# Kernel optimization log

Hardware: AMD Instinct MI355X
Metric: run time of the kernel (lower is better)

## Reference

```python
import jax, jax.numpy as jnp
import numpy as np

N_NODES = 100000
NUM_GRAPHS = 128
FEAT = 128
NUM_CLASSES = 4


def setup_inputs() -> dict:
    key = jax.random.key(0)
    ks = jax.random.split(key, 12)
    x = jax.random.normal(ks[0], (N_NODES, FEAT), dtype=jnp.float32)
    edge_index = jax.random.randint(ks[1], (2, 3200000), 0, N_NODES, dtype=jnp.int64)
    batch = jnp.sort(jax.random.randint(ks[2], (N_NODES,), 0, NUM_GRAPHS, dtype=jnp.int64))

    def glorot(k, fan_in, fan_out):
        lim = float(np.sqrt(6.0 / (fan_in + fan_out)))
        return jax.random.uniform(k, (fan_in, fan_out), jnp.float32, -lim, lim)

    dims = [FEAT, 16, 32, 64, NUM_CLASSES]
    params = {}
    for i in range(4):
        params[f"W{i+1}"] = glorot(ks[3 + i], dims[i], dims[i + 1])
        params[f"b{i+1}"] = jnp.zeros((dims[i + 1],), jnp.float32)
    return dict(x=x, edge_index=edge_index, batch=batch, **params)


def _gcn_norm(edge_index, n):
    # add self-loops, then symmetric normalization deg^{-1/2} A_hat deg^{-1/2}
    loop = jnp.arange(n, dtype=edge_index.dtype)
    row = jnp.concatenate([edge_index[0], loop])  # source
    col = jnp.concatenate([edge_index[1], loop])  # target
    deg = jax.ops.segment_sum(jnp.ones_like(col, jnp.float32), col, num_segments=n)
    dinv = jnp.where(deg > 0, jax.lax.rsqrt(deg), 0.0)
    norm = dinv[row] * dinv[col]  # [E+N]
    return row, col, norm


def _gcn_conv(x, row, col, norm, W, b):
    h = x @ W  # [N, out]
    msg = h[row] * norm[:, None]  # gather + scale, [E+N, out]
    agg = jax.ops.segment_sum(msg, col, num_segments=x.shape[0])
    return agg + b


def reference(x, edge_index, batch, W1, b1, W2, b2, W3, b3, W4, b4):
    n = x.shape[0]
    row, col, norm = _gcn_norm(edge_index, n)
    # dropout is identity in eval mode
    h = jax.nn.relu(_gcn_conv(x, row, col, norm, W1, b1))
    h = jax.nn.relu(_gcn_conv(h, row, col, norm, W2, b2))
    h = jax.nn.relu(_gcn_conv(h, row, col, norm, W3, b3))
    h = _gcn_conv(h, row, col, norm, W4, b4)
    pooled = jax.ops.segment_max(h, batch, num_segments=NUM_GRAPHS)  # [G, C]
    return jax.nn.log_softmax(pooled, axis=1)
```

## Files before the change

kernel.cpp:

```cpp
#include <hip/hip_runtime.h>

#define DIV_UP(a,b) (((a)+(b)-1)/(b))

constexpr int BSHIFT = 7;
constexpr int BNODES = 128;
constexpr int CHUNK_E = 16384;
constexpr int PTH = 512;
constexpr int SCH = 8;
constexpr int SCSH = 14;

__device__ inline unsigned short f2bf(float f) {
    unsigned u = __float_as_uint(f);
    u = u + 0x7FFFu + ((u >> 16) & 1u);
    return (unsigned short)(u >> 16);
}
__device__ inline float bflo(unsigned u) { return __uint_as_float(u << 16); }
__device__ inline float bfhi(unsigned u) { return __uint_as_float(u & 0xFFFF0000u); }

__global__ void zero_int_k(int* p, int n) {
    int i = blockIdx.x * blockDim.x + threadIdx.x;
    if (i < n) p[i] = 0;
}

__global__ void bucket_hist_k(const int* __restrict__ col, int* __restrict__ bhist, int E, int nb) {
    __shared__ int lh[1024];
    for (int i = threadIdx.x; i < 1024; i += blockDim.x) lh[i] = 0;
    __syncthreads();
    int stride = gridDim.x * blockDim.x;
    for (int e = blockIdx.x * blockDim.x + threadIdx.x; e < E; e += stride)
        atomicAdd(&lh[col[e] >> BSHIFT], 1);
    __syncthreads();
    for (int i = threadIdx.x; i < nb; i += blockDim.x) {
        int v = lh[i];
        if (v) atomicAdd(&bhist[i], v);
    }
}

__global__ void bucket_scan_k(const int* __restrict__ bhist, int* __restrict__ bcur, int nb) {
    __shared__ int lds[256];
    int base = threadIdx.x * 4;
    int v[4]; int s = 0;
#pragma unroll
    for (int j = 0; j < 4; j++) { v[j] = (base + j < nb) ? bhist[base + j] : 0; s += v[j]; }
    lds[threadIdx.x] = s; __syncthreads();
    for (int off = 1; off < 256; off <<= 1) {
        int t = (threadIdx.x >= off) ? lds[threadIdx.x - off] : 0;
        __syncthreads();
        lds[threadIdx.x] += t;
        __syncthreads();
    }
    int excl = lds[threadIdx.x] - s;
#pragma unroll
    for (int j = 0; j < 4; j++) {
        if (base + j < nb) bcur[base + j] = excl;
        excl += v[j];
    }
}

__global__ void __launch_bounds__(PTH) partition_k(
        const int* __restrict__ row, const int* __restrict__ col,
        int* __restrict__ bcur, int* __restrict__ part, int E, int nb) {
    __shared__ int lh[1024];
    __shared__ int lbase[1024];
    __shared__ int delta[1024];
    __shared__ unsigned sorted[CHUNK_E];
    __shared__ unsigned short bid[CHUNK_E];
    int tid = threadIdx.x;
    for (int i = tid; i < 1024; i += PTH) lh[i] = 0;
    __syncthreads();
    int base = blockIdx.x * CHUNK_E;
    int end = min(E, base + CHUNK_E);
    for (int e = base + tid; e < end; e += PTH)
        atomicAdd(&lh[col[e] >> BSHIFT], 1);
    __syncthreads();
    int v0 = lh[2 * tid], v1 = lh[2 * tid + 1];
    int s = v0 + v1;
    delta[tid] = s;
    __syncthreads();
    for (int off = 1; off < PTH; off <<= 1) {
        int t = (tid >= off) ? delta[tid - off] : 0;
        __syncthreads();
        delta[tid] += t;
        __syncthreads();
    }
    int excl = delta[tid] - s;
    lbase[2 * tid] = excl;
    lbase[2 * tid + 1] = excl + v0;
    __syncthreads();
    for (int i = tid; i < nb; i += PTH) {
        int c = lh[i];
        int g = c ? atomicAdd(&bcur[i], c) : 0;
        delta[i] = g - lbase[i];
    }
    __syncthreads();
    for (int i = tid; i < nb; i += PTH) lh[i] = lbase[i];
    __syncthreads();
    for (int e = base + tid; e < end; e += PTH) {
        int r = row[e], c = col[e];
        int b = c >> BSHIFT;
        int slot = atomicAdd(&lh[b], 1);
        sorted[slot] = (unsigned)((r << BSHIFT) | (c & (BNODES - 1)));
        bid[slot] = (unsigned short)b;
    }
    __syncthreads();
    int cnt = end - base;
    for (int i = tid; i < cnt; i += PTH) {
        int b = bid[i];
        part[delta[b] + i] = (int)sorted[i];
    }
}

__global__ void __launch_bounds__(256) csr_build_k(
        const int* __restrict__ part, const int* __restrict__ bcur,
        int* __restrict__ cur, float* __restrict__ dinv,
        int* __restrict__ csr, int N) {
    __shared__ int cnt[BNODES * SCH];
    __shared__ int scan_t[256];
    __shared__ int ebounds[2];
    int b = blockIdx.x;
    int tid = threadIdx.x;
    if (tid == 0) { ebounds[0] = b ? bcur[b - 1] : 0; ebounds[1] = bcur[b]; }
    for (int i = tid; i < BNODES * SCH; i += 256) cnt[i] = 0;
    __syncthreads();
    int e0 = ebounds[0], e1 = ebounds[1];
    for (int e = e0 + tid; e < e1; e += 256) {
        unsigned v = (unsigned)part[e];
        int cell = (int)(v & (BNODES - 1)) * SCH + (int)(v >> (BSHIFT + SCSH));
        atomicAdd(&cnt[cell], 1);
    }
    __syncthreads();
    int base4 = tid * 4;
    int c0 = cnt[base4], c1 = cnt[base4+1], c2 = cnt[base4+2], c3 = cnt[base4+3];
    int s = c0 + c1 + c2 + c3;
    scan_t[tid] = s;
    __syncthreads();
    for (int off = 1; off < 256; off <<= 1) {
        int t = (tid >= off) ? scan_t[tid - off] : 0;
        __syncthreads();
        scan_t[tid] += t;
        __syncthreads();
    }
    int excl = scan_t[tid] - s;
    cnt[base4]     = excl;
    cnt[base4 + 1] = excl + c0;
    cnt[base4 + 2] = excl + c0 + c1;
    cnt[base4 + 3] = excl + c0 + c1 + c2;
    __syncthreads();
    if (tid < BNODES) {
        int node = b * BNODES + tid;
        int segstart = cnt[tid * SCH];
        int segend   = (tid == BNODES - 1) ? (e1 - e0) : cnt[(tid + 1) * SCH];
        if (node < N) {
            cur[node]  = e0 + segend;
            dinv[node] = rsqrtf(1.0f + (float)(segend - segstart));
        }
    }
    __syncthreads();
    for (int e = e0 + tid; e < e1; e += 256) {
        unsigned v = (unsigned)part[e];
        int cell = (int)(v & (BNODES - 1)) * SCH + (int)(v >> (BSHIFT + SCSH));
        int p = atomicAdd(&cnt[cell], 1);
        csr[e0 + p] = (int)(v >> BSHIFT);
    }
}

__global__ void __launch_bounds__(256) gather16_bf_k(
        const unsigned short* __restrict__ hb, const float* __restrict__ dinv,
        const int* __restrict__ cur, const int* __restrict__ csr,
        const float* __restrict__ b, unsigned short* __restrict__ outb, int n) {
    int t2 = blockIdx.x * 256 + threadIdx.x;
    int node = t2 >> 1, t = t2 & 1;
    if (node >= n) return;
    const uint4* hb4 = reinterpret_cast<const uint4*>(hb);
    uint4 sv = hb4[(size_t)node * 2 + t];
    float a0 = bflo(sv.x), a1 = bfhi(sv.x), a2 = bflo(sv.y), a3 = bfhi(sv.y);
    float a4 = bflo(sv.z), a5 = bfhi(sv.z), a6 = bflo(sv.w), a7 = bfhi(sv.w);
    int e0 = node ? cur[node - 1] : 0;
    int e1 = cur[node];
    int e = e0;
    for (; e + 3 < e1; e += 4) {
        int s0 = csr[e], s1 = csr[e+1], s2 = csr[e+2], s3 = csr[e+3];
        uint4 v0 = hb4[(size_t)s0 * 2 + t];
        uint4 v1 = hb4[(size_t)s1 * 2 + t];
        uint4 v2 = hb4[(size_t)s2 * 2 + t];
        uint4 v3 = hb4[(size_t)s3 * 2 + t];
        a0 += (bflo(v0.x) + bflo(v1.x)) + (bflo(v2.x) + bflo(v3.x));
        a1 += (bfhi(v0.x) + bfhi(v1.x)) + (bfhi(v2.x) + bfhi(v3.x));
        a2 += (bflo(v0.y) + bflo(v1.y)) + (bflo(v2.y) + bflo(v3.y));
        a3 += (bfhi(v0.y) + bfhi(v1.y)) + (bfhi(v2.y) + bfhi(v3.y));
        a4 += (bflo(v0.z) + bflo(v1.z)) + (bflo(v2.z) + bflo(v3.z));
        a5 += (bfhi(v0.z) + bfhi(v1.z)) + (bfhi(v2.z) + bfhi(v3.z));
        a6 += (bflo(v0.w) + bflo(v1.w)) + (bflo(v2.w) + bflo(v3.w));
        a7 += (bfhi(v0.w) + bfhi(v1.w)) + (bfhi(v2.w) + bfhi(v3.w));
    }
    for (; e < e1; e++) {
        uint4 v = hb4[(size_t)csr[e] * 2 + t];
        a0 += bflo(v.x); a1 += bfhi(v.x); a2 += bflo(v.y); a3 += bfhi(v.y);
        a4 += bflo(v.z); a5 += bfhi(v.z); a6 += bflo(v.w); a7 += bfhi(v.w);
    }
    float di = dinv[node];
    int bo = t * 8;
    a0 = fmaxf(a0 * di + b[bo+0], 0.f) * di; a1 = fmaxf(a1 * di + b[bo+1], 0.f) * di;
    a2 = fmaxf(a2 * di + b[bo+2], 0.f) * di; a3 = fmaxf(a3 * di + b[bo+3], 0.f) * di;
    a4 = fmaxf(a4 * di + b[bo+4], 0.f) * di; a5 = fmaxf(a5 * di + b[bo+5], 0.f) * di;
    a6 = fmaxf(a6 * di + b[bo+6], 0.f) * di; a7 = fmaxf(a7 * di + b[bo+7], 0.f) * di;
    uint4 pk;
    pk.x = (unsigned)f2bf(a0) | ((unsigned)f2bf(a1) << 16);
    pk.y = (unsigned)f2bf(a2) | ((unsigned)f2bf(a3) << 16);
    pk.z = (unsigned)f2bf(a4) | ((unsigned)f2bf(a5) << 16);
    pk.w = (unsigned)f2bf(a6) | ((unsigned)f2bf(a7) << 16);
    reinterpret_cast<uint4*>(outb)[(size_t)node * 2 + t] = pk;
}

__global__ void __launch_bounds__(256) gmm16_32_k(
        const unsigned short* __restrict__ hb, const float* __restrict__ dinv,
        const int* __restrict__ cur, const int* __restrict__ csr,
        const float* __restrict__ W, const float* __restrict__ b,
        unsigned short* __restrict__ yb, int n) {
    constexpr int TN = 128, RS = 20;
    __shared__ float xs[TN * RS];
    __shared__ float Ws[16 * 32];
    __shared__ float bs[32];
    for (int i = threadIdx.x; i < 16 * 32; i += 256) Ws[i] = W[i];
    if (threadIdx.x < 32) bs[threadIdx.x] = b[threadIdx.x];
    int base = blockIdx.x * TN;
    {
        int nl = threadIdx.x >> 1, t = threadIdx.x & 1;
        int node = base + nl;
        if (node < n) {
            const uint4* hb4 = reinterpret_cast<const uint4*>(hb);
            uint4 sv = hb4[(size_t)node * 2 + t];
            float a0 = bflo(sv.x), a1 = bfhi(sv.x), a2 = bflo(sv.y), a3 = bfhi(sv.y);
            float a4 = bflo(sv.z), a5 = bfhi(sv.z), a6 = bflo(sv.w), a7 = bfhi(sv.w);
            int e0 = node ? cur[node - 1] : 0;
            int e1 = cur[node];
            int e = e0;
            for (; e + 3 < e1; e += 4) {
                int s0 = csr[e], s1 = csr[e+1], s2 = csr[e+2], s3 = csr[e+3];
                uint4 v0 = hb4[(size_t)s0 * 2 + t];
                uint4 v1 = hb4[(size_t)s1 * 2 + t];
                uint4 v2 = hb4[(size_t)s2 * 2 + t];
                uint4 v3 = hb4[(size_t)s3 * 2 + t];
                a0 += (bflo(v0.x) + bflo(v1.x)) + (bflo(v2.x) + bflo(v3.x));
                a1 += (bfhi(v0.x) + bfhi(v1.x)) + (bfhi(v2.x) + bfhi(v3.x));
                a2 += (bflo(v0.y) + bflo(v1.y)) + (bflo(v2.y) + bflo(v3.y));
                a3 += (bfhi(v0.y) + bfhi(v1.y)) + (bfhi(v2.y) + bfhi(v3.y));
                a4 += (bflo(v0.z) + bflo(v1.z)) + (bflo(v2.z) + bflo(v3.z));
                a5 += (bfhi(v0.z) + bfhi(v1.z)) + (bfhi(v2.z) + bfhi(v3.z));
                a6 += (bflo(v0.w) + bflo(v1.w)) + (bflo(v2.w) + bflo(v3.w));
                a7 += (bfhi(v0.w) + bfhi(v1.w)) + (bfhi(v2.w) + bfhi(v3.w));
            }
            for (; e < e1; e++) {
                uint4 v = hb4[(size_t)csr[e] * 2 + t];
                a0 += bflo(v.x); a1 += bfhi(v.x); a2 += bflo(v.y); a3 += bfhi(v.y);
                a4 += bflo(v.z); a5 += bfhi(v.z); a6 += bflo(v.w); a7 += bfhi(v.w);
            }
            float di = dinv[node];
            float* dst = &xs[nl * RS + t * 8];
            dst[0] = a0*di; dst[1] = a1*di; dst[2] = a2*di; dst[3] = a3*di;
            dst[4] = a4*di; dst[5] = a5*di; dst[6] = a6*di; dst[7] = a7*di;
        }
    }
    __syncthreads();
    int nl = threadIdx.x >> 1, g = threadIdx.x & 1;
    int node = base + nl;
    if (node >= n) return;
    int j0 = g * 16;
    float acc[16];
#pragma unroll
    for (int j = 0; j < 16; j++) acc[j] = 0.f;
    const float* xrow = &xs[nl * RS];
#pragma unroll
    for (int k4 = 0; k4 < 4; k4++) {
        float4 xv = *reinterpret_cast<const float4*>(&xrow[k4 * 4]);
        float xk[4] = {xv.x, xv.y, xv.z, xv.w};
#pragma unroll
        for (int kk = 0; kk < 4; kk++) {
            const float* wrow = &Ws[(k4*4+kk) * 32 + j0];
#pragma unroll
            for (int j = 0; j < 16; j++) acc[j] += xk[kk] * wrow[j];
        }
    }
    float di = dinv[node];
    unsigned short* yr = yb + (size_t)node * 32 + j0;
#pragma unroll
    for (int q = 0; q < 2; q++) {
        float o[8];
#pragma unroll
        for (int j = 0; j < 8; j++)
            o[j] = fmaxf(acc[q*8+j] + bs[j0 + q*8 + j], 0.f) * di;
        uint4 pk;
        pk.x = (unsigned)f2bf(o[0]) | ((unsigned)f2bf(o[1]) << 16);
        pk.y = (unsigned)f2bf(o[2]) | ((unsigned)f2bf(o[3]) << 16);
        pk.z = (unsigned)f2bf(o[4]) | ((unsigned)f2bf(o[5]) << 16);
        pk.w = (unsigned)f2bf(o[6]) | ((unsigned)f2bf(o[7]) << 16);
        reinterpret_cast<uint4*>(yr)[q] = pk;
    }
}

__global__ void __launch_bounds__(256) gmm32_64_k(
        const unsigned short* __restrict__ hb, const float* __restrict__ dinv,
        const int* __restrict__ cur, const int* __restrict__ csr,
        const float* __restrict__ W, const float* __restrict__ b,
        unsigned short* __restrict__ yb, int n) {
    constexpr int TN = 64, RS = 36;
    __shared__ float xs[TN * RS];
    __shared__ float Ws[32 * 64];
    __shared__ float bs[64];
    for (int i = threadIdx.x; i < 32 * 64; i += 256) Ws[i] = W[i];
    if (threadIdx.x < 64) bs[threadIdx.x] = b[threadIdx.x];
    int base = blockIdx.x * TN;
    {
        int nl = threadIdx.x >> 2, t = threadIdx.x & 3;
        int node = base + nl;
        if (node < n) {
            const uint4* hb4 = reinterpret_cast<const uint4*>(hb);
            uint4 sv = hb4[(size_t)node * 4 + t];
            float a0 = bflo(sv.x), a1 = bfhi(sv.x), a2 = bflo(sv.y), a3 = bfhi(sv.y);
            float a4 = bflo(sv.z), a5 = bfhi(sv.z), a6 = bflo(sv.w), a7 = bfhi(sv.w);
            int e0 = node ? cur[node - 1] : 0;
            int e1 = cur[node];
            int e = e0;
            for (; e + 3 < e1; e += 4) {
                int s0 = csr[e], s1 = csr[e+1], s2 = csr[e+2], s3 = csr[e+3];
                uint4 v0 = hb4[(size_t)s0 * 4 + t];
                uint4 v1 = hb4[(size_t)s1 * 4 + t];
                uint4 v2 = hb4[(size_t)s2 * 4 + t];
                uint4 v3 = hb4[(size_t)s3 * 4 + t];
                a0 += (bflo(v0.x) + bflo(v1.x)) + (bflo(v2.x) + bflo(v3.x));
                a1 += (bfhi(v0.x) + bfhi(v1.x)) + (bfhi(v2.x) + bfhi(v3.x));
                a2 += (bflo(v0.y) + bflo(v1.y)) + (bflo(v2.y) + bflo(v3.y));
                a3 += (bfhi(v0.y) + bfhi(v1.y)) + (bfhi(v2.y) + bfhi(v3.y));
                a4 += (bflo(v0.z) + bflo(v1.z)) + (bflo(v2.z) + bflo(v3.z));
                a5 += (bfhi(v0.z) + bfhi(v1.z)) + (bfhi(v2.z) + bfhi(v3.z));
                a6 += (bflo(v0.w) + bflo(v1.w)) + (bflo(v2.w) + bflo(v3.w));
                a7 += (bfhi(v0.w) + bfhi(v1.w)) + (bfhi(v2.w) + bfhi(v3.w));
            }
            for (; e < e1; e++) {
                uint4 v = hb4[(size_t)csr[e] * 4 + t];
                a0 += bflo(v.x); a1 += bfhi(v.x); a2 += bflo(v.y); a3 += bfhi(v.y);
                a4 += bflo(v.z); a5 += bfhi(v.z); a6 += bflo(v.w); a7 += bfhi(v.w);
            }
            float di = dinv[node];
            float* dst = &xs[nl * RS + t * 8];
            dst[0] = a0*di; dst[1] = a1*di; dst[2] = a2*di; dst[3] = a3*di;
            dst[4] = a4*di; dst[5] = a5*di; dst[6] = a6*di; dst[7] = a7*di;
        }
    }
    __syncthreads();
    int nl = threadIdx.x >> 2, g = threadIdx.x & 3;
    int node = base + nl;
    if (node >= n) return;
    int j0 = g * 16;
    float acc[16];
#pragma unroll
    for (int j = 0; j < 16; j++) acc[j] = 0.f;
    const float* xrow = &xs[nl * RS];
#pragma unroll
    for (int k4 = 0; k4 < 8; k4++) {
        float4 xv = *reinterpret_cast<const float4*>(&xrow[k4 * 4]);
        float xk[4] = {xv.x, xv.y, xv.z, xv.w};
#pragma unroll
        for (int kk = 0; kk < 4; kk++) {
            const float* wrow = &Ws[(k4*4+kk) * 64 + j0];
#pragma unroll
            for (int j = 0; j < 16; j++) acc[j] += xk[kk] * wrow[j];
        }
    }
    float di = dinv[node];
    unsigned short* yr = yb + (size_t)node * 64 + j0;
#pragma unroll
    for (int q = 0; q < 2; q++) {
        float o[8];
#pragma unroll
        for (int j = 0; j < 8; j++)
            o[j] = fmaxf(acc[q*8+j] + bs[j0 + q*8 + j], 0.f) * di;
        uint4 pk;
        pk.x = (unsigned)f2bf(o[0]) | ((unsigned)f2bf(o[1]) << 16);
        pk.y = (unsigned)f2bf(o[2]) | ((unsigned)f2bf(o[3]) << 16);
        pk.z = (unsigned)f2bf(o[4]) | ((unsigned)f2bf(o[5]) << 16);
        pk.w = (unsigned)f2bf(o[6]) | ((unsigned)f2bf(o[7]) << 16);
        reinterpret_cast<uint4*>(yr)[q] = pk;
    }
}

__device__ inline unsigned fkey(float x) {
    unsigned u = __float_as_uint(x);
    return (u & 0x80000000u) ? ~u : (u | 0x80000000u);
}
__device__ inline float funkey(unsigned k) {
    unsigned u = (k & 0x80000000u) ? (k & 0x7FFFFFFFu) : ~k;
    return __uint_as_float(u);
}

__global__ void gather4_pool_k(const float* __restrict__ hs, const float* __restrict__ dinv,
                               const int* __restrict__ cur, const int* __restrict__ csr,
                               const float* __restrict__ b4, const int* __restrict__ batch,
                               unsigned* __restrict__ pooled, int n, int num_graphs) {
    __shared__ unsigned lds[128 * 4];
    for (int i = threadIdx.x; i < num_graphs * 4; i += blockDim.x) lds[i] = 0u;
    __syncthreads();
    int node = blockIdx.x * blockDim.x + threadIdx.x;
    if (node < n) {
        float di = dinv[node];
        float4 acc = reinterpret_cast<const float4*>(hs)[node];
        int e0 = node ? cur[node - 1] : 0;
        int e1 = cur[node];
        int e = e0;
        for (; e + 3 < e1; e += 4) {
            int s0 = csr[e], s1 = csr[e+1], s2 = csr[e+2], s3 = csr[e+3];
            float4 v0 = reinterpret_cast<const float4*>(hs)[s0];
            float4 v1 = reinterpret_cast<const float4*>(hs)[s1];
            float4 v2 = reinterpret_cast<const float4*>(hs)[s2];
            float4 v3 = reinterpret_cast<const float4*>(hs)[s3];
            acc.x += (v0.x + v1.x) + (v2.x + v3.x);
            acc.y += (v0.y + v1.y) + (v2.y + v3.y);
            acc.z += (v0.z + v1.z) + (v2.z + v3.z);
            acc.w += (v0.w + v1.w) + (v2.w + v3.w);
        }
        for (; e < e1; e++) {
            float4 v0 = reinterpret_cast<const float4*>(hs)[csr[e]];
            acc.x += v0.x; acc.y += v0.y; acc.z += v0.z; acc.w += v0.w;
        }
        int g = batch[node];
        atomicMax(&lds[g*4+0], fkey(acc.x * di + b4[0]));
        atomicMax(&lds[g*4+1], fkey(acc.y * di + b4[1]));
        atomicMax(&lds[g*4+2], fkey(acc.z * di + b4[2]));
        atomicMax(&lds[g*4+3], fkey(acc.w * di + b4[3]));
    }
    __syncthreads();
    for (int i2 = threadIdx.x; i2 < num_graphs * 4; i2 += blockDim.x) {
        unsigned k = lds[i2];
        if (k) atomicMax(&pooled[i2], k);
    }
}

__global__ void pool_init_k(unsigned* pooled, int total) {
    int i = blockIdx.x * blockDim.x + threadIdx.x;
    if (i < total) pooled[i] = 0u;
}

__global__ void logsoftmax_k(const unsigned* __restrict__ pooled, float* __restrict__ out, int G) {
    int g = blockIdx.x * blockDim.x + threadIdx.x;
    if (g >= G) return;
    float v[4];
#pragma unroll
    for (int j = 0; j < 4; j++) v[j] = funkey(pooled[g*4+j]);
    float m = fmaxf(fmaxf(v[0], v[1]), fmaxf(v[2], v[3]));
    float s = 0.f;
#pragma unroll
    for (int j = 0; j < 4; j++) s += expf(v[j] - m);
    float l = logf(s);
#pragma unroll
    for (int j = 0; j < 4; j++) out[g*4+j] = v[j] - m - l;
}

template<int IN, int OUT, bool RELU, bool BIAS, bool SCALE, bool IBF, bool OBF>
__global__ void __launch_bounds__(256) matmul_k(
        const void* __restrict__ xv, const float* __restrict__ W,
        const float* __restrict__ b, const float* __restrict__ dinv,
        void* __restrict__ yv, int n) {
    constexpr int TN  = 64;
    constexpr int RS  = IN + 4;
    constexpr int OPT = OUT / 4;
    constexpr int NQ  = IN / 4;
    __shared__ float xs[TN * RS];
    __shared__ float Ws[IN * OUT];
    __shared__ float bs[OUT];

    for (int i = threadIdx.x; i < IN * OUT; i += 256) Ws[i] = W[i];
    if (BIAS) for (int i = threadIdx.x; i < OUT; i += 256) bs[i] = b[i];

    int base = blockIdx.x * TN;
    if constexpr (!IBF) {
        const float* x = (const float*)xv;
        for (int i = threadIdx.x; i < TN * NQ; i += 256) {
            int r = i / NQ, c = i % NQ;
            float4 v = make_float4(0.f, 0.f, 0.f, 0.f);
            if (base + r < n) v = reinterpret_cast<const float4*>(x + (size_t)(base + r) * IN)[c];
            *reinterpret_cast<float4*>(&xs[r * RS + c * 4]) = v;
        }
    } else {
        constexpr int NU = IN / 8;
        const uint4* x = (const uint4*)xv;
        for (int i = threadIdx.x; i < TN * NU; i += 256) {
            int r = i / NU, c = i % NU;
            uint4 v = make_uint4(0u, 0u, 0u, 0u);
            if (base + r < n) v = x[(size_t)(base + r) * NU + c];
            float* dst = &xs[r * RS + c * 8];
            dst[0] = bflo(v.x); dst[1] = bfhi(v.x);
            dst[2] = bflo(v.y); dst[3] = bfhi(v.y);
            dst[4] = bflo(v.z); dst[5] = bfhi(v.z);
            dst[6] = bflo(v.w); dst[7] = bfhi(v.w);
        }
    }
    __syncthreads();

    int node = threadIdx.x >> 2;
    int g    = threadIdx.x & 3;
    int j0   = g * OPT;
    int gnode = base + node;
    if (gnode >= n) return;

    float acc[OPT];
#pragma unroll
    for (int jj = 0; jj < OPT; jj++) acc[jj] = 0.f;

    const float* xrow = &xs[node * RS];
#pragma unroll
    for (int k4 = 0; k4 < NQ; k4++) {
        float4 xvv = *reinterpret_cast<const float4*>(&xrow[k4 * 4]);
        float xk[4] = {xvv.x, xvv.y, xvv.z, xvv.w};
#pragma unroll
        for (int kk = 0; kk < 4; kk++) {
            const float* wrow = &Ws[(k4 * 4 + kk) * OUT + j0];
#pragma unroll
            for (int jj = 0; jj < OPT; jj++)
                acc[jj] += xk[kk] * wrow[jj];
        }
    }

    float di = SCALE ? dinv[gnode] : 1.f;
    float vout[OPT];
#pragma unroll
    for (int jj = 0; jj < OPT; jj++) {
        float v = acc[jj] + (BIAS ? bs[j0 + jj] : 0.f);
        if (RELU) v = fmaxf(v, 0.f);
        if (SCALE) v *= di;
        vout[jj] = v;
    }
    if constexpr (OBF) {
        unsigned short* yr = (unsigned short*)yv + (size_t)gnode * OUT + j0;
        if constexpr (OPT % 8 == 0) {
#pragma unroll
            for (int q = 0; q < OPT / 8; q++) {
                uint4 pk;
                pk.x = (unsigned)f2bf(vout[q*8+0]) | ((unsigned)f2bf(vout[q*8+1]) << 16);
                pk.y = (unsigned)f2bf(vout[q*8+2]) | ((unsigned)f2bf(vout[q*8+3]) << 16);
                pk.z = (unsigned)f2bf(vout[q*8+4]) | ((unsigned)f2bf(vout[q*8+5]) << 16);
                pk.w = (unsigned)f2bf(vout[q*8+6]) | ((unsigned)f2bf(vout[q*8+7]) << 16);
                reinterpret_cast<uint4*>(yr)[q] = pk;
            }
        } else {
            uint2 pk;
            pk.x = (unsigned)f2bf(vout[0]) | ((unsigned)f2bf(vout[1]) << 16);
            pk.y = (unsigned)f2bf(vout[2]) | ((unsigned)f2bf(vout[3]) << 16);
            *reinterpret_cast<uint2*>(yr) = pk;
        }
    } else {
        float* yr = (float*)yv + (size_t)gnode * OUT + j0;
        if (OPT % 4 == 0) {
#pragma unroll
            for (int q = 0; q < OPT / 4; q++)
                *reinterpret_cast<float4*>(yr + q * 4) =
                    make_float4(vout[q*4+0], vout[q*4+1], vout[q*4+2], vout[q*4+3]);
        } else {
#pragma unroll
            for (int jj = 0; jj < OPT; jj++) yr[jj] = vout[jj];
        }
    }
}

extern "C" void kernel_launch(void* const* d_in, const int* in_sizes, int n_in,
                              void* d_out, int out_size, void* d_ws, size_t ws_size,
                              hipStream_t stream) {
    const float* x     = (const float*)d_in[0];
    const int*   ei    = (const int*)d_in[1];
    const int*   batch = (const int*)d_in[2];
    const float* W1 = (const float*)d_in[3];
    const float* b1 = (const float*)d_in[4];
    const float* W2 = (const float*)d_in[5];
    const float* b2 = (const float*)d_in[6];
    const float* W3 = (const float*)d_in[7];
    const float* b3 = (const float*)d_in[8];
    const float* W4 = (const float*)d_in[9];
    const float* b4 = (const float*)d_in[10];

    const int N = in_sizes[2];
    const int E = in_sizes[1] / 2;
    const int G = 128;
    const int* row = ei;
    const int* col = ei + E;
    const int NB = DIV_UP(N, BNODES);

    float* ws    = (float*)d_ws;
    float* dinv  = ws;
    int*   cur   = (int*)(dinv + N);
    int*   bhist = cur + N;
    int*   bcur  = bhist + 1024;
    int*   csr   = bcur + 1024;
    float* f16a  = (float*)(csr + E);
    float* f16b  = f16a + (size_t)N * 16;
    float* f32a  = f16b + (size_t)N * 16;
    float* f32b  = f32a + (size_t)N * 32;
    unsigned* pooled = (unsigned*)(f32b + (size_t)N * 32);
    int* part = (int*)f32a;
    unsigned short* hb16a = (unsigned short*)f16a;
    unsigned short* hb16b = (unsigned short*)f16b;
    unsigned short* hb32  = (unsigned short*)f32a;
    unsigned short* hb64  = (unsigned short*)f32b;
    float* f4a = f16a;

    const int B = 256;
    const int gridN = DIV_UP(N, B);
    const int gridM = DIV_UP(N, 64);
    const int grid2 = DIV_UP(2 * N, B);
    const int gridF = DIV_UP(N, 128);

    zero_int_k<<<DIV_UP(1024, B), B, 0, stream>>>(bhist, 1024);
    bucket_hist_k<<<512, B, 0, stream>>>(col, bhist, E, NB);
    bucket_scan_k<<<1, 256, 0, stream>>>(bhist, bcur, NB);
    partition_k<<<DIV_UP(E, CHUNK_E), PTH, 0, stream>>>(row, col, bcur, part, E, NB);
    csr_build_k<<<NB, 256, 0, stream>>>(part, bcur, cur, dinv, csr, N);

    matmul_k<128,16,false,false,true,false,true><<<gridM, B, 0, stream>>>(x, W1, nullptr, dinv, hb16b, N);
    gather16_bf_k<<<grid2, B, 0, stream>>>(hb16b, dinv, cur, csr, b1, hb16a, N);

    gmm16_32_k<<<gridF, B, 0, stream>>>(hb16a, dinv, cur, csr, W2, b2, hb32, N);

    gmm32_64_k<<<gridM, B, 0, stream>>>(hb32, dinv, cur, csr, W3, b3, hb64, N);

    matmul_k<64,4,false,false,false,true,false><<<gridM, B, 0, stream>>>(hb64, W4, nullptr, nullptr, f4a, N);
    pool_init_k<<<DIV_UP(G*4, B), B, 0, stream>>>(pooled, G*4);
    gather4_pool_k<<<gridN, B, 0, stream>>>(f4a, dinv, cur, csr, b4, batch, pooled, N, G);

    logsoftmax_k<<<1, 128, 0, stream>>>(pooled, (float*)d_out, G);
}
```

Measured before the change: 228.2 us.

## Split each node's edge list across multiple lanes with shuffle reduction in gathers

All four neighbor-aggregation kernels now assign several lanes per node (4x, 2x, 2x and 8x respectively) that stride through the node's edge list and combine partial sums with xor shuffles. This raises the number of independent gather loads in flight and shortens per-thread serial loops, targeting latency-bound random gathers. Node tiles per block are halved in the fused GEMM kernels, and each thread computes 8 output columns instead of 16. The cost is more threads, extra shuffle work, and idle lanes on low-degree nodes.

```diff
diff --git a/kernel.cpp b/kernel.cpp
--- a/kernel.cpp
+++ b/kernel.cpp
@@ -168,22 +168,26 @@
         const unsigned short* __restrict__ hb, const float* __restrict__ dinv,
         const int* __restrict__ cur, const int* __restrict__ csr,
         const float* __restrict__ b, unsigned short* __restrict__ outb, int n) {
-    int t2 = blockIdx.x * 256 + threadIdx.x;
-    int node = t2 >> 1, t = t2 & 1;
+    int tid = blockIdx.x * 256 + threadIdx.x;
+    int node = tid >> 3, sub = tid & 7;
+    int rh = sub & 1, p = sub >> 1;
     if (node >= n) return;
     const uint4* hb4 = reinterpret_cast<const uint4*>(hb);
-    uint4 sv = hb4[(size_t)node * 2 + t];
-    float a0 = bflo(sv.x), a1 = bfhi(sv.x), a2 = bflo(sv.y), a3 = bfhi(sv.y);
-    float a4 = bflo(sv.z), a5 = bfhi(sv.z), a6 = bflo(sv.w), a7 = bfhi(sv.w);
+    float a0 = 0.f, a1 = 0.f, a2 = 0.f, a3 = 0.f, a4 = 0.f, a5 = 0.f, a6 = 0.f, a7 = 0.f;
+    if (p == 0) {
+        uint4 sv = hb4[(size_t)node * 2 + rh];
+        a0 = bflo(sv.x); a1 = bfhi(sv.x); a2 = bflo(sv.y); a3 = bfhi(sv.y);
+        a4 = bflo(sv.z); a5 = bfhi(sv.z); a6 = bflo(sv.w); a7 = bfhi(sv.w);
+    }
     int e0 = node ? cur[node - 1] : 0;
     int e1 = cur[node];
-    int e = e0;
-    for (; e + 3 < e1; e += 4) {
-        int s0 = csr[e], s1 = csr[e+1], s2 = csr[e+2], s3 = csr[e+3];
-        uint4 v0 = hb4[(size_t)s0 * 2 + t];
-        uint4 v1 = hb4[(size_t)s1 * 2 + t];
-        uint4 v2 = hb4[(size_t)s2 * 2 + t];
-        uint4 v3 = hb4[(size_t)s3 * 2 + t];
+    int e = e0 + p;
+    for (; e + 12 < e1; e += 16) {
+        int s0 = csr[e], s1 = csr[e+4], s2 = csr[e+8], s3 = csr[e+12];
+        uint4 v0 = hb4[(size_t)s0 * 2 + rh];
+        uint4 v1 = hb4[(size_t)s1 * 2 + rh];
+        uint4 v2 = hb4[(size_t)s2 * 2 + rh];
+        uint4 v3 = hb4[(size_t)s3 * 2 + rh];
         a0 += (bflo(v0.x) + bflo(v1.x)) + (bflo(v2.x) + bflo(v3.x));
         a1 += (bfhi(v0.x) + bfhi(v1.x)) + (bfhi(v2.x) + bfhi(v3.x));
         a2 += (bflo(v0.y) + bflo(v1.y)) + (bflo(v2.y) + bflo(v3.y));
@@ -193,13 +197,18 @@
         a6 += (bflo(v0.w) + bflo(v1.w)) + (bflo(v2.w) + bflo(v3.w));
         a7 += (bfhi(v0.w) + bfhi(v1.w)) + (bfhi(v2.w) + bfhi(v3.w));
     }
-    for (; e < e1; e++) {
-        uint4 v = hb4[(size_t)csr[e] * 2 + t];
+    for (; e < e1; e += 4) {
+        uint4 v = hb4[(size_t)csr[e] * 2 + rh];
         a0 += bflo(v.x); a1 += bfhi(v.x); a2 += bflo(v.y); a3 += bfhi(v.y);
         a4 += bflo(v.z); a5 += bfhi(v.z); a6 += bflo(v.w); a7 += bfhi(v.w);
     }
+    a0 += __shfl_xor(a0, 2); a1 += __shfl_xor(a1, 2); a2 += __shfl_xor(a2, 2); a3 += __shfl_xor(a3, 2);
+    a4 += __shfl_xor(a4, 2); a5 += __shfl_xor(a5, 2); a6 += __shfl_xor(a6, 2); a7 += __shfl_xor(a7, 2);
+    a0 += __shfl_xor(a0, 4); a1 += __shfl_xor(a1, 4); a2 += __shfl_xor(a2, 4); a3 += __shfl_xor(a3, 4);
+    a4 += __shfl_xor(a4, 4); a5 += __shfl_xor(a5, 4); a6 += __shfl_xor(a6, 4); a7 += __shfl_xor(a7, 4);
+    if (p != 0) return;
     float di = dinv[node];
-    int bo = t * 8;
+    int bo = rh * 8;
     a0 = fmaxf(a0 * di + b[bo+0], 0.f) * di; a1 = fmaxf(a1 * di + b[bo+1], 0.f) * di;
     a2 = fmaxf(a2 * di + b[bo+2], 0.f) * di; a3 = fmaxf(a3 * di + b[bo+3], 0.f) * di;
     a4 = fmaxf(a4 * di + b[bo+4], 0.f) * di; a5 = fmaxf(a5 * di + b[bo+5], 0.f) * di;
@@ -209,7 +218,7 @@
     pk.y = (unsigned)f2bf(a2) | ((unsigned)f2bf(a3) << 16);
     pk.z = (unsigned)f2bf(a4) | ((unsigned)f2bf(a5) << 16);
     pk.w = (unsigned)f2bf(a6) | ((unsigned)f2bf(a7) << 16);
-    reinterpret_cast<uint4*>(outb)[(size_t)node * 2 + t] = pk;
+    reinterpret_cast<uint4*>(outb)[(size_t)node * 2 + rh] = pk;
 }
 
 __global__ void __launch_bounds__(256) gmm16_32_k(
@@ -217,7 +226,7 @@
         const int* __restrict__ cur, const int* __restrict__ csr,
         const float* __restrict__ W, const float* __restrict__ b,
         unsigned short* __restrict__ yb, int n) {
-    constexpr int TN = 128, RS = 20;
+    constexpr int TN = 64, RS = 20;
     __shared__ float xs[TN * RS];
     __shared__ float Ws[16 * 32];
     __shared__ float bs[32];
@@ -225,22 +234,26 @@
     if (threadIdx.x < 32) bs[threadIdx.x] = b[threadIdx.x];
     int base = blockIdx.x * TN;
     {
-        int nl = threadIdx.x >> 1, t = threadIdx.x & 1;
+        int nl = threadIdx.x >> 2, sub = threadIdx.x & 3;
+        int rh = sub & 1, p = sub >> 1;
         int node = base + nl;
         if (node < n) {
             const uint4* hb4 = reinterpret_cast<const uint4*>(hb);
-            uint4 sv = hb4[(size_t)node * 2 + t];
-            float a0 = bflo(sv.x), a1 = bfhi(sv.x), a2 = bflo(sv.y), a3 = bfhi(sv.y);
-            float a4 = bflo(sv.z), a5 = bfhi(sv.z), a6 = bflo(sv.w), a7 = bfhi(sv.w);
+            float a0 = 0.f, a1 = 0.f, a2 = 0.f, a3 = 0.f, a4 = 0.f, a5 = 0.f, a6 = 0.f, a7 = 0.f;
+            if (p == 0) {
+                uint4 sv = hb4[(size_t)node * 2 + rh];
+                a0 = bflo(sv.x); a1 = bfhi(sv.x); a2 = bflo(sv.y); a3 = bfhi(sv.y);
+                a4 = bflo(sv.z); a5 = bfhi(sv.z); a6 = bflo(sv.w); a7 = bfhi(sv.w);
+            }
             int e0 = node ? cur[node - 1] : 0;
             int e1 = cur[node];
-            int e = e0;
-            for (; e + 3 < e1; e += 4) {
-                int s0 = csr[e], s1 = csr[e+1], s2 = csr[e+2], s3 = csr[e+3];
-                uint4 v0 = hb4[(size_t)s0 * 2 + t];
-                uint4 v1 = hb4[(size_t)s1 * 2 + t];
-                uint4 v2 = hb4[(size_t)s2 * 2 + t];
-                uint4 v3 = hb4[(size_t)s3 * 2 + t];
+            int e = e0 + p;
+            for (; e + 6 < e1; e += 8) {
+                int s0 = csr[e], s1 = csr[e+2], s2 = csr[e+4], s3 = csr[e+6];
+                uint4 v0 = hb4[(size_t)s0 * 2 + rh];
+                uint4 v1 = hb4[(size_t)s1 * 2 + rh];
+                uint4 v2 = hb4[(size_t)s2 * 2 + rh];
+                uint4 v3 = hb4[(size_t)s3 * 2 + rh];
                 a0 += (bflo(v0.x) + bflo(v1.x)) + (bflo(v2.x) + bflo(v3.x));
                 a1 += (bfhi(v0.x) + bfhi(v1.x)) + (bfhi(v2.x) + bfhi(v3.x));
                 a2 += (bflo(v0.y) + bflo(v1.y)) + (bflo(v2.y) + bflo(v3.y));
@@ -250,25 +263,29 @@
                 a6 += (bflo(v0.w) + bflo(v1.w)) + (bflo(v2.w) + bflo(v3.w));
                 a7 += (bfhi(v0.w) + bfhi(v1.w)) + (bfhi(v2.w) + bfhi(v3.w));
             }
-            for (; e < e1; e++) {
-                uint4 v = hb4[(size_t)csr[e] * 2 + t];
+            for (; e < e1; e += 2) {
+                uint4 v = hb4[(size_t)csr[e] * 2 + rh];
                 a0 += bflo(v.x); a1 += bfhi(v.x); a2 += bflo(v.y); a3 += bfhi(v.y);
                 a4 += bflo(v.z); a5 += bfhi(v.z); a6 += bflo(v.w); a7 += bfhi(v.w);
             }
-            float di = dinv[node];
-            float* dst = &xs[nl * RS + t * 8];
-            dst[0] = a0*di; dst[1] = a1*di; dst[2] = a2*di; dst[3] = a3*di;
-            dst[4] = a4*di; dst[5] = a5*di; dst[6] = a6*di; dst[7] = a7*di;
-        }
-    }
-    __syncthreads();
-    int nl = threadIdx.x >> 1, g = threadIdx.x & 1;
+            a0 += __shfl_xor(a0, 2); a1 += __shfl_xor(a1, 2); a2 += __shfl_xor(a2, 2); a3 += __shfl_xor(a3, 2);
+            a4 += __shfl_xor(a4, 2); a5 += __shfl_xor(a5, 2); a6 += __shfl_xor(a6, 2); a7 += __shfl_xor(a7, 2);
+            if (p == 0) {
+                float di = dinv[node];
+                float* dst = &xs[nl * RS + rh * 8];
+                dst[0] = a0*di; dst[1] = a1*di; dst[2] = a2*di; dst[3] = a3*di;
+                dst[4] = a4*di; dst[5] = a5*di; dst[6] = a6*di; dst[7] = a7*di;
+            }
+        }
+    }
+    __syncthreads();
+    int nl = threadIdx.x >> 2, g = threadIdx.x & 3;
     int node = base + nl;
     if (node >= n) return;
-    int j0 = g * 16;
-    float acc[16];
-#pragma unroll
-    for (int j = 0; j < 16; j++) acc[j] = 0.f;
+    int j0 = g * 8;
+    float acc[8];
+#pragma unroll
+    for (int j = 0; j < 8; j++) acc[j] = 0.f;
     const float* xrow = &xs[nl * RS];
 #pragma unroll
     for (int k4 = 0; k4 < 4; k4++) {
@@ -278,24 +295,19 @@
         for (int kk = 0; kk < 4; kk++) {
             const float* wrow = &Ws[(k4*4+kk) * 32 + j0];
 #pragma unroll
-            for (int j = 0; j < 16; j++) acc[j] += xk[kk] * wrow[j];
+            for (int j = 0; j < 8; j++) acc[j] += xk[kk] * wrow[j];
         }
     }
     float di = dinv[node];
-    unsigned short* yr = yb + (size_t)node * 32 + j0;
-#pragma unroll
-    for (int q = 0; q < 2; q++) {
-        float o[8];
-#pragma unroll
-        for (int j = 0; j < 8; j++)
-            o[j] = fmaxf(acc[q*8+j] + bs[j0 + q*8 + j], 0.f) * di;
-        uint4 pk;
-        pk.x = (unsigned)f2bf(o[0]) | ((unsigned)f2bf(o[1]) << 16);
-        pk.y = (unsigned)f2bf(o[2]) | ((unsigned)f2bf(o[3]) << 16);
-        pk.z = (unsigned)f2bf(o[4]) | ((unsigned)f2bf(o[5]) << 16);
-        pk.w = (unsigned)f2bf(o[6]) | ((unsigned)f2bf(o[7]) << 16);
-        reinterpret_cast<uint4*>(yr)[q] = pk;
-    }
+    float o[8];
+#pragma unroll
+    for (int j = 0; j < 8; j++) o[j] = fmaxf(acc[j] + bs[j0 + j], 0.f) * di;
+    uint4 pk;
+    pk.x = (unsigned)f2bf(o[0]) | ((unsigned)f2bf(o[1]) << 16);
+    pk.y = (unsigned)f2bf(o[2]) | ((unsigned)f2bf(o[3]) << 16);
+    pk.z = (unsigned)f2bf(o[4]) | ((unsigned)f2bf(o[5]) << 16);
+    pk.w = (unsigned)f2bf(o[6]) | ((unsigned)f2bf(o[7]) << 16);
+    *reinterpret_cast<uint4*>(yb + (size_t)node * 32 + j0) = pk;
 }
 
 __global__ void __launch_bounds__(256) gmm32_64_k(
@@ -303,7 +315,7 @@
         const int* __restrict__ cur, const int* __restrict__ csr,
         const float* __restrict__ W, const float* __restrict__ b,
         unsigned short* __restrict__ yb, int n) {
-    constexpr int TN = 64, RS = 36;
+    constexpr int TN = 32, RS = 36;
     __shared__ float xs[TN * RS];
     __shared__ float Ws[32 * 64];
     __shared__ float bs[64];
@@ -311,22 +323,26 @@
     if (threadIdx.x < 64) bs[threadIdx.x] = b[threadIdx.x];
     int base = blockIdx.x * TN;
     {
-        int nl = threadIdx.x >> 2, t = threadIdx.x & 3;
+        int nl = threadIdx.x >> 3, sub = threadIdx.x & 7;
+        int rq = sub & 3, p = sub >> 2;
         int node = base + nl;
         if (node < n) {
             const uint4* hb4 = reinterpret_cast<const uint4*>(hb);
-            uint4 sv = hb4[(size_t)node * 4 + t];
-            float a0 = bflo(sv.x), a1 = bfhi(sv.x), a2 = bflo(sv.y), a3 = bfhi(sv.y);
-            float a4 = bflo(sv.z), a5 = bfhi(sv.z), a6 = bflo(sv.w), a7 = bfhi(sv.w);
+            float a0 = 0.f, a1 = 0.f, a2 = 0.f, a3 = 0.f, a4 = 0.f, a5 = 0.f, a6 = 0.f, a7 = 0.f;
+            if (p == 0) {
+                uint4 sv = hb4[(size_t)node * 4 + rq];
+                a0 = bflo(sv.x); a1 = bfhi(sv.x); a2 = bflo(sv.y); a3 = bfhi(sv.y);
+                a4 = bflo(sv.z); a5 = bfhi(sv.z); a6 = bflo(sv.w); a7 = bfhi(sv.w);
+            }
             int e0 = node ? cur[node - 1] : 0;
             int e1 = cur[node];
-            int e = e0;
-            for (; e + 3 < e1; e += 4) {
-                int s0 = csr[e], s1 = csr[e+1], s2 = csr[e+2], s3 = csr[e+3];
-                uint4 v0 = hb4[(size_t)s0 * 4 + t];
-                uint4 v1 = hb4[(size_t)s1 * 4 + t];
-                uint4 v2 = hb4[(size_t)s2 * 4 + t];
-                uint4 v3 = hb4[(size_t)s3 * 4 + t];
+            int e = e0 + p;
+            for (; e + 6 < e1; e += 8) {
+                int s0 = csr[e], s1 = csr[e+2], s2 = csr[e+4], s3 = csr[e+6];
+                uint4 v0 = hb4[(size_t)s0 * 4 + rq];
+                uint4 v1 = hb4[(size_t)s1 * 4 + rq];
+                uint4 v2 = hb4[(size_t)s2 * 4 + rq];
+                uint4 v3 = hb4[(size_t)s3 * 4 + rq];
                 a0 += (bflo(v0.x) + bflo(v1.x)) + (bflo(v2.x) + bflo(v3.x));
                 a1 += (bfhi(v0.x) + bfhi(v1.x)) + (bfhi(v2.x) + bfhi(v3.x));
                 a2 += (bflo(v0.y) + bflo(v1.y)) + (bflo(v2.y) + bflo(v3.y));
@@ -336,25 +352,29 @@
                 a6 += (bflo(v0.w) + bflo(v1.w)) + (bflo(v2.w) + bflo(v3.w));
                 a7 += (bfhi(v0.w) + bfhi(v1.w)) + (bfhi(v2.w) + bfhi(v3.w));
             }
-            for (; e < e1; e++) {
-                uint4 v = hb4[(size_t)csr[e] * 4 + t];
+            for (; e < e1; e += 2) {
+                uint4 v = hb4[(size_t)csr[e] * 4 + rq];
                 a0 += bflo(v.x); a1 += bfhi(v.x); a2 += bflo(v.y); a3 += bfhi(v.y);
                 a4 += bflo(v.z); a5 += bfhi(v.z); a6 += bflo(v.w); a7 += bfhi(v.w);
             }
-            float di = dinv[node];
-            float* dst = &xs[nl * RS + t * 8];
-            dst[0] = a0*di; dst[1] = a1*di; dst[2] = a2*di; dst[3] = a3*di;
-            dst[4] = a4*di; dst[5] = a5*di; dst[6] = a6*di; dst[7] = a7*di;
-        }
-    }
-    __syncthreads();
-    int nl = threadIdx.x >> 2, g = threadIdx.x & 3;
+            a0 += __shfl_xor(a0, 4); a1 += __shfl_xor(a1, 4); a2 += __shfl_xor(a2, 4); a3 += __shfl_xor(a3, 4);
+            a4 += __shfl_xor(a4, 4); a5 += __shfl_xor(a5, 4); a6 += __shfl_xor(a6, 4); a7 += __shfl_xor(a7, 4);
+            if (p == 0) {
+                float di = dinv[node];
+                float* dst = &xs[nl * RS + rq * 8];
+                dst[0] = a0*di; dst[1] = a1*di; dst[2] = a2*di; dst[3] = a3*di;
+                dst[4] = a4*di; dst[5] = a5*di; dst[6] = a6*di; dst[7] = a7*di;
+            }
+        }
+    }
+    __syncthreads();
+    int nl = threadIdx.x >> 3, g = threadIdx.x & 7;
     int node = base + nl;
     if (node >= n) return;
-    int j0 = g * 16;
-    float acc[16];
-#pragma unroll
-    for (int j = 0; j < 16; j++) acc[j] = 0.f;
+    int j0 = g * 8;
+    float acc[8];
+#pragma unroll
+    for (int j = 0; j < 8; j++) acc[j] = 0.f;
     const float* xrow = &xs[nl * RS];
 #pragma unroll
     for (int k4 = 0; k4 < 8; k4++) {
@@ -364,24 +384,19 @@
         for (int kk = 0; kk < 4; kk++) {
             const float* wrow = &Ws[(k4*4+kk) * 64 + j0];
 #pragma unroll
-            for (int j = 0; j < 16; j++) acc[j] += xk[kk] * wrow[j];
+            for (int j = 0; j < 8; j++) acc[j] += xk[kk] * wrow[j];
         }
     }
     float di = dinv[node];
-    unsigned short* yr = yb + (size_t)node * 64 + j0;
-#pragma unroll
-    for (int q = 0; q < 2; q++) {
-        float o[8];
-#pragma unroll
-        for (int j = 0; j < 8; j++)
-            o[j] = fmaxf(acc[q*8+j] + bs[j0 + q*8 + j], 0.f) * di;
-        uint4 pk;
-        pk.x = (unsigned)f2bf(o[0]) | ((unsigned)f2bf(o[1]) << 16);
-        pk.y = (unsigned)f2bf(o[2]) | ((unsigned)f2bf(o[3]) << 16);
-        pk.z = (unsigned)f2bf(o[4]) | ((unsigned)f2bf(o[5]) << 16);
-        pk.w = (unsigned)f2bf(o[6]) | ((unsigned)f2bf(o[7]) << 16);
-        reinterpret_cast<uint4*>(yr)[q] = pk;
-    }
+    float o[8];
+#pragma unroll
+    for (int j = 0; j < 8; j++) o[j] = fmaxf(acc[j] + bs[j0 + j], 0.f) * di;
+    uint4 pk;
+    pk.x = (unsigned)f2bf(o[0]) | ((unsigned)f2bf(o[1]) << 16);
+    pk.y = (unsigned)f2bf(o[2]) | ((unsigned)f2bf(o[3]) << 16);
+    pk.z = (unsigned)f2bf(o[4]) | ((unsigned)f2bf(o[5]) << 16);
+    pk.w = (unsigned)f2bf(o[6]) | ((unsigned)f2bf(o[7]) << 16);
+    *reinterpret_cast<uint4*>(yb + (size_t)node * 64 + j0) = pk;
 }
 
 __device__ inline unsigned fkey(float x) {
@@ -400,33 +415,39 @@
     __shared__ unsigned lds[128 * 4];
     for (int i = threadIdx.x; i < num_graphs * 4; i += blockDim.x) lds[i] = 0u;
     __syncthreads();
-    int node = blockIdx.x * blockDim.x + threadIdx.x;
+    int tid = blockIdx.x * blockDim.x + threadIdx.x;
+    int node = tid >> 3, p = tid & 7;
     if (node < n) {
-        float di = dinv[node];
-        float4 acc = reinterpret_cast<const float4*>(hs)[node];
+        float4 acc = make_float4(0.f, 0.f, 0.f, 0.f);
+        if (p == 0) acc = reinterpret_cast<const float4*>(hs)[node];
         int e0 = node ? cur[node - 1] : 0;
         int e1 = cur[node];
-        int e = e0;
-        for (; e + 3 < e1; e += 4) {
-            int s0 = csr[e], s1 = csr[e+1], s2 = csr[e+2], s3 = csr[e+3];
-            float4 v0 = reinterpret_cast<const float4*>(hs)[s0];
-            float4 v1 = reinterpret_cast<const float4*>(hs)[s1];
-            float4 v2 = reinterpret_cast<const float4*>(hs)[s2];
-            float4 v3 = reinterpret_cast<const float4*>(hs)[s3];
-            acc.x += (v0.x + v1.x) + (v2.x + v3.x);
-            acc.y += (v0.y + v1.y) + (v2.y + v3.y);
-            acc.z += (v0.z + v1.z) + (v2.z + v3.z);
-            acc.w += (v0.w + v1.w) + (v2.w + v3.w);
-        }
-        for (; e < e1; e++) {
+        int e = e0 + p;
+        for (; e + 8 < e1; e += 16) {
+            float4 v0 = reinterpret_cast<const float4*>(hs)[csr[e]];
+            float4 v1 = reinterpret_cast<const float4*>(hs)[csr[e + 8]];
+            acc.x += v0.x + v1.x; acc.y += v0.y + v1.y;
+            acc.z += v0.z + v1.z; acc.w += v0.w + v1.w;
+        }
+        for (; e < e1; e += 8) {
             float4 v0 = reinterpret_cast<const float4*>(hs)[csr[e]];
             acc.x += v0.x; acc.y += v0.y; acc.z += v0.z; acc.w += v0.w;
         }
-        int g = batch[node];
-        atomicMax(&lds[g*4+0], fkey(acc.x * di + b4[0]));
-        atomicMax(&lds[g*4+1], fkey(acc.y * di + b4[1]));
-        atomicMax(&lds[g*4+2], fkey(acc.z * di + b4[2]));
-        atomicMax(&lds[g*4+3], fkey(acc.w * di + b4[3]));
+#pragma unroll
+        for (int m = 1; m <= 4; m <<= 1) {
+            acc.x += __shfl_xor(acc.x, m);
+            acc.y += __shfl_xor(acc.y, m);
+            acc.z += __shfl_xor(acc.z, m);
+            acc.w += __shfl_xor(acc.w, m);
+        }
+        if (p == 0) {
+            float di = dinv[node];
+            int g = batch[node];
+            atomicMax(&lds[g*4+0], fkey(acc.x * di + b4[0]));
+            atomicMax(&lds[g*4+1], fkey(acc.y * di + b4[1]));
+            atomicMax(&lds[g*4+2], fkey(acc.z * di + b4[2]));
+            atomicMax(&lds[g*4+3], fkey(acc.w * di + b4[3]));
+        }
     }
     __syncthreads();
     for (int i2 = threadIdx.x; i2 < num_graphs * 4; i2 += blockDim.x) {
@@ -602,10 +623,9 @@
     float* f4a = f16a;
 
     const int B = 256;
-    const int gridN = DIV_UP(N, B);
-    const int gridM = DIV_UP(N, 64);
-    const int grid2 = DIV_UP(2 * N, B);
-    const int gridF = DIV_UP(N, 128);
+    const int gridM  = DIV_UP(N, 64);
+    const int grid32 = DIV_UP(N, 32);
+    const int grid8  = DIV_UP(8 * N, B);
 
     zero_int_k<<<DIV_UP(1024, B), B, 0, stream>>>(bhist, 1024);
     bucket_hist_k<<<512, B, 0, stream>>>(col, bhist, E, NB);
@@ -614,15 +634,15 @@
     csr_build_k<<<NB, 256, 0, stream>>>(part, bcur, cur, dinv, csr, N);
 
     matmul_k<128,16,false,false,true,false,true><<<gridM, B, 0, stream>>>(x, W1, nullptr, dinv, hb16b, N);
-    gather16_bf_k<<<grid2, B, 0, stream>>>(hb16b, dinv, cur, csr, b1, hb16a, N);
-
-    gmm16_32_k<<<gridF, B, 0, stream>>>(hb16a, dinv, cur, csr, W2, b2, hb32, N);
-
-    gmm32_64_k<<<gridM, B, 0, stream>>>(hb32, dinv, cur, csr, W3, b3, hb64, N);
+    gather16_bf_k<<<grid8, B, 0, stream>>>(hb16b, dinv, cur, csr, b1, hb16a, N);
+
+    gmm16_32_k<<<gridM, B, 0, stream>>>(hb16a, dinv, cur, csr, W2, b2, hb32, N);
+
+    gmm32_64_k<<<grid32, B, 0, stream>>>(hb32, dinv, cur, csr, W3, b3, hb64, N);
 
     matmul_k<64,4,false,false,false,true,false><<<gridM, B, 0, stream>>>(hb64, W4, nullptr, nullptr, f4a, N);
     pool_init_k<<<DIV_UP(G*4, B), B, 0, stream>>>(pooled, G*4);
-    gather4_pool_k<<<gridN, B, 0, stream>>>(f4a, dinv, cur, csr, b4, batch, pooled, N, G);
+    gather4_pool_k<<<grid8, B, 0, stream>>>(f4a, dinv, cur, csr, b4, batch, pooled, N, G);
 
     logsoftmax_k<<<1, 128, 0, stream>>>(pooled, (float*)d_out, G);
 }
```

Result: faster. 218.5 us (median of 2 runs) (-4.2%).
